# Kernel tuning notes

Hardware: AMD Instinct MI355X
Metric: run time of the kernel (lower is better)

Reference implementation:

```python
import jax, jax.numpy as jnp
import numpy as np

SIZE = (128, 160, 128)  # (D, H, W)
BATCH, CHANNELS = 4, 1


def setup_inputs() -> dict:
    key = jax.random.key(0)
    k1, k2 = jax.random.split(key)
    src = jax.random.normal(k1, (BATCH, CHANNELS) + SIZE, dtype=jnp.float32)
    # near-identity affine [B, 3, 4] so most sampled coords land in-volume
    eye = jnp.concatenate([jnp.eye(3, dtype=jnp.float32), jnp.zeros((3, 1), jnp.float32)], axis=1)
    affine_matrix = eye[None] + 0.05 * jax.random.normal(k2, (BATCH, 3, 4), dtype=jnp.float32)
    return {"src": src, "affine_matrix": affine_matrix}


def _mesh_matrix(D, H, W):
    # rows: dim0 (D), dim1 (H), dim2 (W), ones  -> [4, N]
    gz, gy, gx = jnp.meshgrid(jnp.arange(D), jnp.arange(H), jnp.arange(W), indexing='ij')
    N = D * H * W
    return jnp.stack([gz.reshape(N), gy.reshape(N), gx.reshape(N),
                      jnp.ones((N,), jnp.int32)], axis=0).astype(jnp.float32)


def _trilinear_border(src, ix, iy, iz):
    # src: [B, C, D, H, W]; ix/iy/iz: [B, N] unnormalized pixel coords (x->W, y->H, z->D)
    B, C, D, H, W = src.shape
    # border padding: clamp coordinate before interpolation (matches PyTorch)
    ix = jnp.clip(ix, 0.0, W - 1.0)
    iy = jnp.clip(iy, 0.0, H - 1.0)
    iz = jnp.clip(iz, 0.0, D - 1.0)
    x0f, y0f, z0f = jnp.floor(ix), jnp.floor(iy), jnp.floor(iz)
    wx = (ix - x0f)[:, None, :]  # [B,1,N]
    wy = (iy - y0f)[:, None, :]
    wz = (iz - z0f)[:, None, :]
    x0 = x0f.astype(jnp.int32); x1 = jnp.minimum(x0 + 1, W - 1)
    y0 = y0f.astype(jnp.int32); y1 = jnp.minimum(y0 + 1, H - 1)
    z0 = z0f.astype(jnp.int32); z1 = jnp.minimum(z0 + 1, D - 1)
    flat = src.reshape(B, C, D * H * W)
    N = ix.shape[-1]

    def gather(zz, yy, xx):
        idx = (zz * H + yy) * W + xx  # [B, N]
        idx = jnp.broadcast_to(idx[:, None, :], (B, C, N))
        return jnp.take_along_axis(flat, idx, axis=2)  # [B, C, N]

    c000 = gather(z0, y0, x0); c001 = gather(z0, y0, x1)
    c010 = gather(z0, y1, x0); c011 = gather(z0, y1, x1)
    c100 = gather(z1, y0, x0); c101 = gather(z1, y0, x1)
    c110 = gather(z1, y1, x0); c111 = gather(z1, y1, x1)
    c00 = c000 + (c001 - c000) * wx
    c01 = c010 + (c011 - c010) * wx
    c10 = c100 + (c101 - c100) * wx
    c11 = c110 + (c111 - c110) * wx
    c0 = c00 + (c01 - c00) * wy
    c1 = c10 + (c11 - c10) * wy
    return c0 + (c1 - c0) * wz  # [B, C, N]


def reference(src, affine_matrix):
    D, H, W = SIZE
    B, C = src.shape[:2]
    mesh = _mesh_matrix(D, H, W)  # [4, N]
    loc = jnp.einsum('bij,jn->bin', affine_matrix, mesh)  # [B, 3, N] voxel coords
    sizes = jnp.array([D, H, W], jnp.float32)
    g = 2.0 * (loc / (sizes[None, :, None] - 1.0) - 0.5)  # normalized, dims (d0,d1,d2)
    # flip to grid_sample (x, y, z) ordering, then unnormalize (align_corners=False)
    ix = ((g[:, 2] + 1.0) * W - 1.0) * 0.5
    iy = ((g[:, 1] + 1.0) * H - 1.0) * 0.5
    iz = ((g[:, 0] + 1.0) * D - 1.0) * 0.5
    out = _trilinear_border(src, ix, iy, iz)  # [B, C, N]
    return out.reshape(B, C, D, H, W)
```

## Files before the change

### kernel.cpp

```cpp
#include <hip/hip_runtime.h>

#define DD 128
#define HH 160
#define WW 128
#define BB 4
#define HW  20480
#define DHW 2621440

#define TX 64
#define TY 8
#define TZ 4
#define YT (HH / TY)
#define ZT (DD / TZ)
#define NWG (2 * YT * ZT * BB)
#define NXCD 8
#define CPX (NWG / NXCD)
#define LDSF 12800
#define MAXCH (LDSF / 4)

typedef float f2 __attribute__((ext_vector_type(2), aligned(4)));
typedef float v2 __attribute__((ext_vector_type(2)));

__global__ __launch_bounds__(256)
void st_affine_kernel(const float* __restrict__ src,
                      const float* __restrict__ aff,
                      float* __restrict__ out) {
    __shared__ float lds[LDSF];

    const int wgid = blockIdx.x;
    const int lin  = (wgid & (NXCD - 1)) * CPX + (wgid >> 3);
    const int xt = lin & 1;
    const int l2 = lin >> 1;
    const int yt = l2 % YT;
    const int l3 = l2 / YT;
    const int zt = l3 & (ZT - 1);
    const int b  = l3 >> 5;
    const int x0t = xt * TX, y0t = yt * TY, z0t = zt * TZ;

    const float* A = aff + b * 12;
    const float cD = 128.f / 127.f, cH = 160.f / 159.f, cW = 128.f / 127.f;
    const float pz0 = A[0] * cD, pz1 = A[1] * cD, pz2 = A[2]  * cD, pz3 = fmaf(A[3],  cD, -0.5f);
    const float py0 = A[4] * cH, py1 = A[5] * cH, py2 = A[6]  * cH, py3 = fmaf(A[7],  cH, -0.5f);
    const float px0 = A[8] * cW, px1 = A[9] * cW, px2 = A[10] * cW, px3 = fmaf(A[11], cW, -0.5f);

    float mnx = 1e30f, mxx = -1e30f, mny = 1e30f, mxy = -1e30f, mnz = 1e30f, mxz = -1e30f;
#pragma unroll
    for (int ci = 0; ci < 8; ++ci) {
        float czc = (float)(z0t + ((ci & 1) ? TZ - 1 : 0));
        float cyc = (float)(y0t + ((ci & 2) ? TY - 1 : 0));
        float cxc = (float)(x0t + ((ci & 4) ? TX - 1 : 0));
        float iz = fmaf(pz0, czc, fmaf(pz1, cyc, fmaf(pz2, cxc, pz3)));
        float iy = fmaf(py0, czc, fmaf(py1, cyc, fmaf(py2, cxc, py3)));
        float ix = fmaf(px0, czc, fmaf(px1, cyc, fmaf(px2, cxc, px3)));
        mnz = fminf(mnz, iz); mxz = fmaxf(mxz, iz);
        mny = fminf(mny, iy); mxy = fmaxf(mxy, iy);
        mnx = fminf(mnx, ix); mxx = fmaxf(mxx, ix);
    }
    mnx = __builtin_amdgcn_fmed3f(mnx, 0.f, 127.f); mxx = __builtin_amdgcn_fmed3f(mxx, 0.f, 127.f);
    mny = __builtin_amdgcn_fmed3f(mny, 0.f, 159.f); mxy = __builtin_amdgcn_fmed3f(mxy, 0.f, 159.f);
    mnz = __builtin_amdgcn_fmed3f(mnz, 0.f, 127.f); mxz = __builtin_amdgcn_fmed3f(mxz, 0.f, 127.f);
    const int xlo = max(0, (int)floorf(mnx) - 1);
    const int ylo = max(0, (int)floorf(mny) - 1);
    const int zlo = max(0, (int)floorf(mnz) - 1);
    const int xhi = min(WW - 2, (int)floorf(mxx) + 1);
    const int yhi = min(HH - 2, (int)floorf(mxy) + 1);
    const int zhi = min(DD - 2, (int)floorf(mxz) + 1);

    const int xlo4  = xlo & ~3;
    const int XE4   = xhi - xlo4 + 2;
    const int YE    = yhi - ylo + 2;
    const int ZE    = zhi - zlo + 2;
    const int pitch = (XE4 + 3) & ~3;
    const int cpr   = pitch >> 2;
    const int nRows = YE * ZE;
    const int slice = YE * pitch;
    const int spp   = slice + pitch;
    const int totalChunks = nRows * cpr;
    const bool fits = (totalChunks <= MAXCH);

    const int tid  = threadIdx.x;
    const int lane = tid & 63;
    const int wid  = tid >> 6;

    const int xp = x0t + ((lane & 31) << 1);
    const int yo = y0t + (wid << 1) + (lane >> 5);
    const float fx0 = (float)xp, fx1 = (float)(xp + 1);
    const float fy = (float)yo, fz = (float)z0t;

    const float izb0 = fmaf(pz0, fz, fmaf(pz1, fy, fmaf(pz2, fx0, pz3)));
    const float izb1 = fmaf(pz0, fz, fmaf(pz1, fy, fmaf(pz2, fx1, pz3)));
    const float iyb0 = fmaf(py0, fz, fmaf(py1, fy, fmaf(py2, fx0, py3)));
    const float iyb1 = fmaf(py0, fz, fmaf(py1, fy, fmaf(py2, fx1, py3)));
    const float ixb0 = fmaf(px0, fz, fmaf(px1, fy, fmaf(px2, fx0, px3)));
    const float ixb1 = fmaf(px0, fz, fmaf(px1, fy, fmaf(px2, fx1, px3)));

    if (fits) {
        const float rcpr = 1.0f / (float)cpr;
        const float rYE  = 1.0f / (float)YE;
        const float cprF = (float)cpr, YEf = (float)YE;
        const float zloF = (float)zlo, yloF = (float)ylo, xlo4F = (float)xlo4;
        const float* sb = src + b * DHW;
        const int nIt = (totalChunks + 255) >> 8;
        for (int it = 0; it < nIt; ++it) {
            const int k = (it << 8) + (wid << 6) + lane;
            if (k < totalChunks) {
                float kf   = (float)k;
                float rowf = floorf(fmaf(kf, rcpr, 0.5f * rcpr));
                float xif  = fmaf(-rowf, cprF, kf);
                float zif  = floorf(fmaf(rowf, rYE, 0.5f * rYE));
                float yif  = fmaf(-zif, YEf, rowf);
                float gf   = fmaf(zloF + zif, 20480.f,
                             fmaf(yloF + yif, 128.f,
                             fmaf(xif, 4.f, xlo4F)));
                int g = min((int)gf, DHW - 4);
                __builtin_amdgcn_global_load_lds(
                    (const __attribute__((address_space(1))) void*)(sb + g),
                    (__attribute__((address_space(3))) void*)(lds + (size_t)(((it << 8) + (wid << 6)) << 2)),
                    16, 0, 0);
            }
        }
    }
    __syncthreads();

    const float zloF = (float)zlo, yloF = (float)ylo, xlo4F = (float)xlo4;
    const float YEf = (float)YE, pitchF = (float)pitch;

    float* dst = out + (size_t)(((b * DD + z0t) * HH + yo) * WW + xp);

    if (fits) {
        auto sampL = [&](float iz, float iy, float ix) -> float {
            iz = __builtin_amdgcn_fmed3f(iz, 0.f, 127.f);
            iy = __builtin_amdgcn_fmed3f(iy, 0.f, 159.f);
            ix = __builtin_amdgcn_fmed3f(ix, 0.f, 127.f);
            float z0 = fminf(floorf(iz), 126.f);
            float y0 = fminf(floorf(iy), 158.f);
            float x0 = fminf(floorf(ix), 126.f);
            float wz = iz - z0, wy = iy - y0, wx = ix - x0;
            int o = (int)fmaf(fmaf(z0 - zloF, YEf, y0 - yloF), pitchF, x0 - xlo4F);
            f2 v00 = *(const f2*)(lds + o);
            f2 v01 = *(const f2*)(lds + o + pitch);
            f2 v10 = *(const f2*)(lds + o + slice);
            f2 v11 = *(const f2*)(lds + o + spp);
            float c00 = fmaf(v00.y - v00.x, wx, v00.x);
            float c01 = fmaf(v01.y - v01.x, wx, v01.x);
            float c10 = fmaf(v10.y - v10.x, wx, v10.x);
            float c11 = fmaf(v11.y - v11.x, wx, v11.x);
            float c0 = fmaf(c01 - c00, wy, c00);
            float c1 = fmaf(c11 - c10, wy, c10);
            return fmaf(c1 - c0, wz, c0);
        };
#pragma unroll
        for (int k = 0; k < TZ; ++k) {
            const float kf = (float)k;
            v2 r;
            r.x = sampL(fmaf(kf, pz0, izb0), fmaf(kf, py0, iyb0), fmaf(kf, px0, ixb0));
            r.y = sampL(fmaf(kf, pz0, izb1), fmaf(kf, py0, iyb1), fmaf(kf, px0, ixb1));
            __builtin_nontemporal_store(r, (v2*)(dst + k * HW));
        }
    } else {
        const float* sb = src + b * DHW;
        auto sampG = [&](float iz, float iy, float ix) -> float {
            iz = __builtin_amdgcn_fmed3f(iz, 0.f, 127.f);
            iy = __builtin_amdgcn_fmed3f(iy, 0.f, 159.f);
            ix = __builtin_amdgcn_fmed3f(ix, 0.f, 127.f);
            float z0 = fminf(floorf(iz), 126.f);
            float y0 = fminf(floorf(iy), 158.f);
            float x0 = fminf(floorf(ix), 126.f);
            float wz = iz - z0, wy = iy - y0, wx = ix - x0;
            int o = (int)fmaf(z0, 20480.f, fmaf(y0, 128.f, x0));
            const float* p = sb + o;
            f2 v00 = *(const f2*)(p);
            f2 v01 = *(const f2*)(p + WW);
            f2 v10 = *(const f2*)(p + HW);
            f2 v11 = *(const f2*)(p + HW + WW);
            float c00 = fmaf(v00.y - v00.x, wx, v00.x);
            float c01 = fmaf(v01.y - v01.x, wx, v01.x);
            float c10 = fmaf(v10.y - v10.x, wx, v10.x);
            float c11 = fmaf(v11.y - v11.x, wx, v11.x);
            float c0 = fmaf(c01 - c00, wy, c00);
            float c1 = fmaf(c11 - c10, wy, c10);
            return fmaf(c1 - c0, wz, c0);
        };
#pragma unroll
        for (int k = 0; k < TZ; ++k) {
            const float kf = (float)k;
            v2 r;
            r.x = sampG(fmaf(kf, pz0, izb0), fmaf(kf, py0, iyb0), fmaf(kf, px0, ixb0));
            r.y = sampG(fmaf(kf, pz0, izb1), fmaf(kf, py0, iyb1), fmaf(kf, px0, ixb1));
            __builtin_nontemporal_store(r, (v2*)(dst + k * HW));
        }
    }
}

extern "C" void kernel_launch(void* const* d_in, const int* in_sizes, int n_in,
                              void* d_out, int out_size, void* d_ws, size_t ws_size,
                              hipStream_t stream) {
    const float* src = (const float*)d_in[0];
    const float* aff = (const float*)d_in[1];
    float* out = (float*)d_out;

    st_affine_kernel<<<dim3(NWG), dim3(256), 0, stream>>>(src, aff, out);
}
```

Measured before the change: 28.45 us.

## Retile to 32x16x4 with 512 threads, analytic bounds, interior fast path

Reshapes the workgroup tile from 64x8x4 to 32x16x4 with 512 threads per block, so each thread computes 2 z-slices instead of 4. Computes the tile's source bounding box analytically from center plus abs-weighted half extents instead of evaluating 8 corners, and adds an interior flag that skips per-sample clamping. The LDS staging loop drops its per-chunk bounds guard, relying on the index clamp and on a special case that forces the global path for the last batch's far corner tile. This should cut per-thread ALU work and produce a more cubic footprint, but it adds block size and register pressure and the unguarded loads may read past the staged region.

```diff
diff --git a/kernel.cpp b/kernel.cpp
--- a/kernel.cpp
+++ b/kernel.cpp
@@ -7,21 +7,22 @@
 #define HW  20480
 #define DHW 2621440
 
-#define TX 64
-#define TY 8
+#define TX 32
+#define TY 16
 #define TZ 4
+#define XT (WW / TX)
 #define YT (HH / TY)
 #define ZT (DD / TZ)
-#define NWG (2 * YT * ZT * BB)
+#define NWG (XT * YT * ZT * BB)
 #define NXCD 8
 #define CPX (NWG / NXCD)
-#define LDSF 12800
+#define LDSF 10240
 #define MAXCH (LDSF / 4)
 
 typedef float f2 __attribute__((ext_vector_type(2), aligned(4)));
 typedef float v2 __attribute__((ext_vector_type(2)));
 
-__global__ __launch_bounds__(256)
+__global__ __launch_bounds__(512)
 void st_affine_kernel(const float* __restrict__ src,
                       const float* __restrict__ aff,
                       float* __restrict__ out) {
@@ -29,42 +30,43 @@
 
     const int wgid = blockIdx.x;
     const int lin  = (wgid & (NXCD - 1)) * CPX + (wgid >> 3);
-    const int xt = lin & 1;
-    const int l2 = lin >> 1;
+    const int xt = lin & 3;
+    const int l2 = lin >> 2;
     const int yt = l2 % YT;
     const int l3 = l2 / YT;
-    const int zt = l3 & (ZT - 1);
+    const int zt = l3 & 31;
     const int b  = l3 >> 5;
     const int x0t = xt * TX, y0t = yt * TY, z0t = zt * TZ;
 
     const float* A = aff + b * 12;
-    const float cD = 128.f / 127.f, cH = 160.f / 159.f, cW = 128.f / 127.f;
-    const float pz0 = A[0] * cD, pz1 = A[1] * cD, pz2 = A[2]  * cD, pz3 = fmaf(A[3],  cD, -0.5f);
-    const float py0 = A[4] * cH, py1 = A[5] * cH, py2 = A[6]  * cH, py3 = fmaf(A[7],  cH, -0.5f);
-    const float px0 = A[8] * cW, px1 = A[9] * cW, px2 = A[10] * cW, px3 = fmaf(A[11], cW, -0.5f);
-
-    float mnx = 1e30f, mxx = -1e30f, mny = 1e30f, mxy = -1e30f, mnz = 1e30f, mxz = -1e30f;
-#pragma unroll
-    for (int ci = 0; ci < 8; ++ci) {
-        float czc = (float)(z0t + ((ci & 1) ? TZ - 1 : 0));
-        float cyc = (float)(y0t + ((ci & 2) ? TY - 1 : 0));
-        float cxc = (float)(x0t + ((ci & 4) ? TX - 1 : 0));
-        float iz = fmaf(pz0, czc, fmaf(pz1, cyc, fmaf(pz2, cxc, pz3)));
-        float iy = fmaf(py0, czc, fmaf(py1, cyc, fmaf(py2, cxc, py3)));
-        float ix = fmaf(px0, czc, fmaf(px1, cyc, fmaf(px2, cxc, px3)));
-        mnz = fminf(mnz, iz); mxz = fmaxf(mxz, iz);
-        mny = fminf(mny, iy); mxy = fmaxf(mxy, iy);
-        mnx = fminf(mnx, ix); mxx = fmaxf(mxx, ix);
-    }
-    mnx = __builtin_amdgcn_fmed3f(mnx, 0.f, 127.f); mxx = __builtin_amdgcn_fmed3f(mxx, 0.f, 127.f);
-    mny = __builtin_amdgcn_fmed3f(mny, 0.f, 159.f); mxy = __builtin_amdgcn_fmed3f(mxy, 0.f, 159.f);
-    mnz = __builtin_amdgcn_fmed3f(mnz, 0.f, 127.f); mxz = __builtin_amdgcn_fmed3f(mxz, 0.f, 127.f);
-    const int xlo = max(0, (int)floorf(mnx) - 1);
-    const int ylo = max(0, (int)floorf(mny) - 1);
-    const int zlo = max(0, (int)floorf(mnz) - 1);
-    const int xhi = min(WW - 2, (int)floorf(mxx) + 1);
-    const int yhi = min(HH - 2, (int)floorf(mxy) + 1);
-    const int zhi = min(DD - 2, (int)floorf(mxz) + 1);
+    const float cD = 128.f/127.f, cH = 160.f/159.f, cW = 128.f/127.f;
+    const float pz0 = A[0]*cD, pz1 = A[1]*cD, pz2 = A[2]*cD,  pz3 = fmaf(A[3],  cD, -0.5f);
+    const float py0 = A[4]*cH, py1 = A[5]*cH, py2 = A[6]*cH,  py3 = fmaf(A[7],  cH, -0.5f);
+    const float px0 = A[8]*cW, px1 = A[9]*cW, px2 = A[10]*cW, px3 = fmaf(A[11], cW, -0.5f);
+
+    const float hz = (TZ - 1) * 0.5f, hy = (TY - 1) * 0.5f, hx = (TX - 1) * 0.5f;
+    const float ccz = (float)z0t + hz, ccy = (float)y0t + hy, ccx = (float)x0t + hx;
+    const float izc = fmaf(pz0, ccz, fmaf(pz1, ccy, fmaf(pz2, ccx, pz3)));
+    const float iyc = fmaf(py0, ccz, fmaf(py1, ccy, fmaf(py2, ccx, py3)));
+    const float ixc = fmaf(px0, ccz, fmaf(px1, ccy, fmaf(px2, ccx, px3)));
+    const float rz = fmaf(fabsf(pz0), hz, fmaf(fabsf(pz1), hy, fmaf(fabsf(pz2), hx, 1e-3f)));
+    const float ry = fmaf(fabsf(py0), hz, fmaf(fabsf(py1), hy, fmaf(fabsf(py2), hx, 1e-3f)));
+    const float rx = fmaf(fabsf(px0), hz, fmaf(fabsf(px1), hy, fmaf(fabsf(px2), hx, 1e-3f)));
+    const float mnz = izc - rz, mxz = izc + rz;
+    const float mny = iyc - ry, mxy = iyc + ry;
+    const float mnx = ixc - rx, mxx = ixc + rx;
+
+    const bool interior =
+        (mnz > 0.02f) && (mxz < 126.98f) &&
+        (mny > 0.02f) && (mxy < 158.98f) &&
+        (mnx > 0.02f) && (mxx < 126.98f);
+
+    const int xlo = max(0, (int)floorf(__builtin_amdgcn_fmed3f(mnx, 0.f, 127.f)) - 1);
+    const int ylo = max(0, (int)floorf(__builtin_amdgcn_fmed3f(mny, 0.f, 159.f)) - 1);
+    const int zlo = max(0, (int)floorf(__builtin_amdgcn_fmed3f(mnz, 0.f, 127.f)) - 1);
+    const int xhi = min(WW - 2, (int)floorf(__builtin_amdgcn_fmed3f(mxx, 0.f, 127.f)) + 1);
+    const int yhi = min(HH - 2, (int)floorf(__builtin_amdgcn_fmed3f(mxy, 0.f, 159.f)) + 1);
+    const int zhi = min(DD - 2, (int)floorf(__builtin_amdgcn_fmed3f(mxz, 0.f, 127.f)) + 1);
 
     const int xlo4  = xlo & ~3;
     const int XE4   = xhi - xlo4 + 2;
@@ -72,123 +74,121 @@
     const int ZE    = zhi - zlo + 2;
     const int pitch = (XE4 + 3) & ~3;
     const int cpr   = pitch >> 2;
-    const int nRows = YE * ZE;
     const int slice = YE * pitch;
-    const int spp   = slice + pitch;
-    const int totalChunks = nRows * cpr;
-    const bool fits = (totalChunks <= MAXCH);
+    const int totalChunks = ZE * YE * cpr;
+
+    bool fits = (totalChunks <= MAXCH);
+    if (b == BB - 1 && zhi >= DD - 3 && yhi >= HH - 3 && xhi >= WW - 7) fits = false;
 
     const int tid  = threadIdx.x;
     const int lane = tid & 63;
     const int wid  = tid >> 6;
 
-    const int xp = x0t + ((lane & 31) << 1);
-    const int yo = y0t + (wid << 1) + (lane >> 5);
-    const float fx0 = (float)xp, fx1 = (float)(xp + 1);
-    const float fy = (float)yo, fz = (float)z0t;
-
-    const float izb0 = fmaf(pz0, fz, fmaf(pz1, fy, fmaf(pz2, fx0, pz3)));
-    const float izb1 = fmaf(pz0, fz, fmaf(pz1, fy, fmaf(pz2, fx1, pz3)));
-    const float iyb0 = fmaf(py0, fz, fmaf(py1, fy, fmaf(py2, fx0, py3)));
-    const float iyb1 = fmaf(py0, fz, fmaf(py1, fy, fmaf(py2, fx1, py3)));
-    const float ixb0 = fmaf(px0, fz, fmaf(px1, fy, fmaf(px2, fx0, px3)));
-    const float ixb1 = fmaf(px0, fz, fmaf(px1, fy, fmaf(px2, fx1, px3)));
-
     if (fits) {
-        const float rcpr = 1.0f / (float)cpr;
-        const float rYE  = 1.0f / (float)YE;
-        const float cprF = (float)cpr, YEf = (float)YE;
+        const float rcpr = 1.f / (float)cpr, rYE = 1.f / (float)YE;
+        const float cprF = (float)cpr, YEfS = (float)YE;
         const float zloF = (float)zlo, yloF = (float)ylo, xlo4F = (float)xlo4;
         const float* sb = src + b * DHW;
-        const int nIt = (totalChunks + 255) >> 8;
+        const int nIt = (totalChunks + 511) >> 9;
         for (int it = 0; it < nIt; ++it) {
-            const int k = (it << 8) + (wid << 6) + lane;
-            if (k < totalChunks) {
-                float kf   = (float)k;
-                float rowf = floorf(fmaf(kf, rcpr, 0.5f * rcpr));
-                float xif  = fmaf(-rowf, cprF, kf);
-                float zif  = floorf(fmaf(rowf, rYE, 0.5f * rYE));
-                float yif  = fmaf(-zif, YEf, rowf);
-                float gf   = fmaf(zloF + zif, 20480.f,
-                             fmaf(yloF + yif, 128.f,
-                             fmaf(xif, 4.f, xlo4F)));
-                int g = min((int)gf, DHW - 4);
-                __builtin_amdgcn_global_load_lds(
-                    (const __attribute__((address_space(1))) void*)(sb + g),
-                    (__attribute__((address_space(3))) void*)(lds + (size_t)(((it << 8) + (wid << 6)) << 2)),
-                    16, 0, 0);
-            }
+            const int k = (it << 9) + tid;
+            float kf   = (float)k;
+            float rowf = floorf(fmaf(kf, rcpr, 0.5f * rcpr));
+            float xif  = fmaf(-rowf, cprF, kf);
+            float zif  = floorf(fmaf(rowf, rYE, 0.5f * rYE));
+            float yif  = fmaf(-zif, YEfS, rowf);
+            float gf   = fmaf(zloF + zif, 20480.f,
+                         fmaf(yloF + yif, 128.f,
+                         fmaf(xif, 4.f, xlo4F)));
+            int g = min((int)gf, DHW - 4);
+            __builtin_amdgcn_global_load_lds(
+                (const __attribute__((address_space(1))) void*)(sb + g),
+                (__attribute__((address_space(3))) void*)(lds + (size_t)(((it << 9) + (wid << 6)) * 4)),
+                16, 0, 0);
         }
     }
     __syncthreads();
 
+    const int xp = x0t + ((lane & 15) << 1);
+    const int yo = y0t + ((lane >> 4) | ((wid & 3) << 2));
+    const int zb = z0t + ((wid >> 2) << 1);
+    const float fx0 = (float)xp, fy = (float)yo, fzb = (float)zb;
+
+    const float izb0 = fmaf(pz0, fzb, fmaf(pz1, fy, fmaf(pz2, fx0, pz3)));
+    const float iyb0 = fmaf(py0, fzb, fmaf(py1, fy, fmaf(py2, fx0, py3)));
+    const float ixb0 = fmaf(px0, fzb, fmaf(px1, fy, fmaf(px2, fx0, px3)));
+    const float izb1 = izb0 + pz2, iyb1 = iyb0 + py2, ixb1 = ixb0 + px2;
+
     const float zloF = (float)zlo, yloF = (float)ylo, xlo4F = (float)xlo4;
     const float YEf = (float)YE, pitchF = (float)pitch;
-
-    float* dst = out + (size_t)(((b * DD + z0t) * HH + yo) * WW + xp);
-
-    if (fits) {
-        auto sampL = [&](float iz, float iy, float ix) -> float {
-            iz = __builtin_amdgcn_fmed3f(iz, 0.f, 127.f);
-            iy = __builtin_amdgcn_fmed3f(iy, 0.f, 159.f);
-            ix = __builtin_amdgcn_fmed3f(ix, 0.f, 127.f);
-            float z0 = fminf(floorf(iz), 126.f);
-            float y0 = fminf(floorf(iy), 158.f);
-            float x0 = fminf(floorf(ix), 126.f);
-            float wz = iz - z0, wy = iy - y0, wx = ix - x0;
-            int o = (int)fmaf(fmaf(z0 - zloF, YEf, y0 - yloF), pitchF, x0 - xlo4F);
-            f2 v00 = *(const f2*)(lds + o);
-            f2 v01 = *(const f2*)(lds + o + pitch);
-            f2 v10 = *(const f2*)(lds + o + slice);
-            f2 v11 = *(const f2*)(lds + o + spp);
-            float c00 = fmaf(v00.y - v00.x, wx, v00.x);
-            float c01 = fmaf(v01.y - v01.x, wx, v01.x);
-            float c10 = fmaf(v10.y - v10.x, wx, v10.x);
-            float c11 = fmaf(v11.y - v11.x, wx, v11.x);
-            float c0 = fmaf(c01 - c00, wy, c00);
-            float c1 = fmaf(c11 - c10, wy, c10);
-            return fmaf(c1 - c0, wz, c0);
-        };
+    float* dst = out + (size_t)(((b * DD + zb) * HH + yo) * WW + xp);
+
+    auto lerpL = [&](int o, float wxs, float wys, float wzs) -> float {
+        f2 v00 = *(const f2*)(lds + o);
+        f2 v01 = *(const f2*)(lds + o + pitch);
+        f2 v10 = *(const f2*)(lds + o + slice);
+        f2 v11 = *(const f2*)(lds + o + slice + pitch);
+        float c00 = fmaf(v00.y - v00.x, wxs, v00.x);
+        float c01 = fmaf(v01.y - v01.x, wxs, v01.x);
+        float c10 = fmaf(v10.y - v10.x, wxs, v10.x);
+        float c11 = fmaf(v11.y - v11.x, wxs, v11.x);
+        float c0 = fmaf(c01 - c00, wys, c00);
+        float c1 = fmaf(c11 - c10, wys, c10);
+        return fmaf(c1 - c0, wzs, c0);
+    };
+    auto lerpG = [&](float cz, float cy, float cx, float wxs, float wys, float wzs) -> float {
+        int o = (int)fmaf(cz, 20480.f, fmaf(cy, 128.f, cx));
+        const float* p = src + b * DHW + o;
+        f2 v00 = *(const f2*)(p);
+        f2 v01 = *(const f2*)(p + WW);
+        f2 v10 = *(const f2*)(p + HW);
+        f2 v11 = *(const f2*)(p + HW + WW);
+        float c00 = fmaf(v00.y - v00.x, wxs, v00.x);
+        float c01 = fmaf(v01.y - v01.x, wxs, v01.x);
+        float c10 = fmaf(v10.y - v10.x, wxs, v10.x);
+        float c11 = fmaf(v11.y - v11.x, wxs, v11.x);
+        float c0 = fmaf(c01 - c00, wys, c00);
+        float c1 = fmaf(c11 - c10, wys, c10);
+        return fmaf(c1 - c0, wzs, c0);
+    };
+
 #pragma unroll
-        for (int k = 0; k < TZ; ++k) {
-            const float kf = (float)k;
-            v2 r;
-            r.x = sampL(fmaf(kf, pz0, izb0), fmaf(kf, py0, iyb0), fmaf(kf, px0, ixb0));
-            r.y = sampL(fmaf(kf, pz0, izb1), fmaf(kf, py0, iyb1), fmaf(kf, px0, ixb1));
-            __builtin_nontemporal_store(r, (v2*)(dst + k * HW));
+    for (int kq = 0; kq < 2; ++kq) {
+        const float kf = (float)kq;
+        float iz0 = fmaf(kf, pz0, izb0), iz1 = fmaf(kf, pz0, izb1);
+        float iy0 = fmaf(kf, py0, iyb0), iy1 = fmaf(kf, py0, iyb1);
+        float ix0 = fmaf(kf, px0, ixb0), ix1 = fmaf(kf, px0, ixb1);
+        float cz0, cy0, cx0, cz1, cy1, cx1;
+        if (interior) {
+            cz0 = floorf(iz0); cz1 = floorf(iz1);
+            cy0 = floorf(iy0); cy1 = floorf(iy1);
+            cx0 = floorf(ix0); cx1 = floorf(ix1);
+        } else {
+            iz0 = __builtin_amdgcn_fmed3f(iz0, 0.f, 127.f);
+            iz1 = __builtin_amdgcn_fmed3f(iz1, 0.f, 127.f);
+            iy0 = __builtin_amdgcn_fmed3f(iy0, 0.f, 159.f);
+            iy1 = __builtin_amdgcn_fmed3f(iy1, 0.f, 159.f);
+            ix0 = __builtin_amdgcn_fmed3f(ix0, 0.f, 127.f);
+            ix1 = __builtin_amdgcn_fmed3f(ix1, 0.f, 127.f);
+            cz0 = fminf(floorf(iz0), 126.f); cz1 = fminf(floorf(iz1), 126.f);
+            cy0 = fminf(floorf(iy0), 158.f); cy1 = fminf(floorf(iy1), 158.f);
+            cx0 = fminf(floorf(ix0), 126.f); cx1 = fminf(floorf(ix1), 126.f);
         }
-    } else {
-        const float* sb = src + b * DHW;
-        auto sampG = [&](float iz, float iy, float ix) -> float {
-            iz = __builtin_amdgcn_fmed3f(iz, 0.f, 127.f);
-            iy = __builtin_amdgcn_fmed3f(iy, 0.f, 159.f);
-            ix = __builtin_amdgcn_fmed3f(ix, 0.f, 127.f);
-            float z0 = fminf(floorf(iz), 126.f);
-            float y0 = fminf(floorf(iy), 158.f);
-            float x0 = fminf(floorf(ix), 126.f);
-            float wz = iz - z0, wy = iy - y0, wx = ix - x0;
-            int o = (int)fmaf(z0, 20480.f, fmaf(y0, 128.f, x0));
-            const float* p = sb + o;
-            f2 v00 = *(const f2*)(p);
-            f2 v01 = *(const f2*)(p + WW);
-            f2 v10 = *(const f2*)(p + HW);
-            f2 v11 = *(const f2*)(p + HW + WW);
-            float c00 = fmaf(v00.y - v00.x, wx, v00.x);
-            float c01 = fmaf(v01.y - v01.x, wx, v01.x);
-            float c10 = fmaf(v10.y - v10.x, wx, v10.x);
-            float c11 = fmaf(v11.y - v11.x, wx, v11.x);
-            float c0 = fmaf(c01 - c00, wy, c00);
-            float c1 = fmaf(c11 - c10, wy, c10);
-            return fmaf(c1 - c0, wz, c0);
-        };
-#pragma unroll
-        for (int k = 0; k < TZ; ++k) {
-            const float kf = (float)k;
-            v2 r;
-            r.x = sampG(fmaf(kf, pz0, izb0), fmaf(kf, py0, iyb0), fmaf(kf, px0, ixb0));
-            r.y = sampG(fmaf(kf, pz0, izb1), fmaf(kf, py0, iyb1), fmaf(kf, px0, ixb1));
-            __builtin_nontemporal_store(r, (v2*)(dst + k * HW));
+        const float wz0 = iz0 - cz0, wz1 = iz1 - cz1;
+        const float wy0 = iy0 - cy0, wy1 = iy1 - cy1;
+        const float wx0 = ix0 - cx0, wx1 = ix1 - cx1;
+
+        v2 r;
+        if (fits) {
+            int o0 = (int)fmaf(fmaf(cz0 - zloF, YEf, cy0 - yloF), pitchF, cx0 - xlo4F);
+            int o1 = (int)fmaf(fmaf(cz1 - zloF, YEf, cy1 - yloF), pitchF, cx1 - xlo4F);
+            r.x = lerpL(o0, wx0, wy0, wz0);
+            r.y = lerpL(o1, wx1, wy1, wz1);
+        } else {
+            r.x = lerpG(cz0, cy0, cx0, wx0, wy0, wz0);
+            r.y = lerpG(cz1, cy1, cx1, wx1, wy1, wz1);
         }
+        __builtin_nontemporal_store(r, (v2*)(dst + kq * HW));
     }
 }
 
@@ -199,5 +199,5 @@
     const float* aff = (const float*)d_in[1];
     float* out = (float*)d_out;
 
-    st_affine_kernel<<<dim3(NWG), dim3(256), 0, stream>>>(src, aff, out);
+    st_affine_kernel<<<dim3(NWG), dim3(512), 0, stream>>>(src, aff, out);
 }
```

Measured after the change: 28.01 us. No clear change (-1.5%).
